# Kernel tuning notes

Measured on AMD Instinct MI355X. Metric: run time of the kernel, lower is better.

The kernel has to match this reference:

```python
import jax, jax.numpy as jnp
import numpy as np

TGT_LEN = 1024
MEM_LEN = 1024
SAME_LENGTH = True
D_MODEL = 2048
BATCH = 4


def _make_ft_real(tgt_len: int, mem_len: int, same_length: bool) -> jnp.ndarray:
    """Build the banded Fourier mixing matrix. Since the module's input x is real
    and only .real of the output is returned, Re(FT @ x) == Re(FT) @ x, so we
    precompute only the real part (this also matches the kernel-headroom note:
    the imaginary output is never used)."""
    qlen = tgt_len
    klen = tgt_len + mem_len
    flen = klen - qlen + 1
    m = np.outer(np.arange(qlen), np.arange(flen))
    ft = np.exp(2j * np.pi * m / flen) / np.sqrt(flen)  # [qlen, flen] complex
    ft = np.pad(ft, ((0, 0), (klen - flen, 0)))          # left-pad to [qlen, klen]
    for i in range(qlen):  # setup-time numpy loop over fixed qlen rows (not traced)
        ft[i] = np.roll(ft[i], -(qlen - i - 1))
    ft = np.tril(ft, klen - qlen)
    if same_length:
        ft = np.triu(ft, 0)
    return jnp.asarray(ft.real.astype(np.float32))


_FT_REAL = _make_ft_real(TGT_LEN, MEM_LEN, SAME_LENGTH)  # [tgt_len, tgt_len+mem_len]


def setup_inputs() -> dict:
    key = jax.random.key(0)
    k1, k2 = jax.random.split(key)
    klen = TGT_LEN + MEM_LEN
    x = jax.random.normal(k1, (BATCH, klen, D_MODEL), dtype=jnp.float32)
    p = jax.random.normal(k2, (BATCH, klen, D_MODEL), dtype=jnp.float32)
    return {"x": x, "p": p, "qlen": TGT_LEN, "add_position": 1}


def reference(x, p, qlen, add_position):
    # Dropout is identity in eval mode (deterministic reference).
    if add_position:
        x = x + p
    klen = x.shape[1]
    ft = _FT_REAL[-qlen:, -klen:]                    # [qlen, klen]
    scale = np.float32(1.0 / np.sqrt(klen))
    # Banded token-mixing matmul; real part only (x is real).
    out = jnp.einsum("lm,bmd->bld", ft, x) * scale   # [B, qlen, D]
    return out
```

## Files before the change

### kernel.cpp

```cpp
#include <hip/hip_runtime.h>
#include <hip/hip_bf16.h>
#include <cstdint>

#define QLEN   1024
#define KLEN   2048
#define DMODEL 2048
#define BATCH  4
#define FLEN   (KLEN - QLEN + 1)

typedef __bf16 bf16x8 __attribute__((ext_vector_type(8)));
typedef __bf16 bf16x4 __attribute__((ext_vector_type(4)));
typedef float  f32x4  __attribute__((ext_vector_type(4)));

__device__ __bf16 g_ft[(size_t)QLEN * KLEN];
__device__ __bf16 g_yt[(size_t)BATCH * DMODEL * KLEN];

typedef __attribute__((address_space(1))) void gvoid;
typedef __attribute__((address_space(3))) void svoid;

__device__ __forceinline__ void async_load16(const void* g, void* lds) {
  gvoid* gp = (gvoid*)(uintptr_t)g;
  svoid* sp = (svoid*)(uint32_t)(uintptr_t)lds;
  __builtin_amdgcn_global_load_lds(gp, sp, 16, 0, 0);
}

__global__ void gen_ft_kernel() {
  const int u  = blockIdx.x * 256 + threadIdx.x;
  const int l  = u >> 8;
  const int m0 = (u & 255) * 8;
  const int j0 = m0 - l;
  bf16x8 o = {};
  if (j0 + 7 >= 0 && j0 < FLEN) {
    const float w     = 6.283185307179586f / (float)FLEN;
    const float scale = 1.0f / sqrtf((float)FLEN * (float)KLEN);
#pragma unroll
    for (int i = 0; i < 8; ++i) {
      const int j = j0 + i;
      float v = 0.0f;
      if (j >= 0 && j < FLEN) {
        const int r = (l * j) % FLEN;
        v = cosf((float)r * w) * scale;
      }
      o[i] = (__bf16)v;
    }
  }
  *(bf16x8*)(g_ft + (size_t)u * 8) = o;
}

__global__ __launch_bounds__(256) void gen_yt_kernel(const float* __restrict__ x,
                                                     const float* __restrict__ p,
                                                     const int* __restrict__ addp) {
  __shared__ __align__(16) float xt[64 * 64];
  __shared__ __align__(16) float pt[64 * 64];
  const int b  = blockIdx.z;
  const int m0 = blockIdx.x * 64;
  const int d0 = blockIdx.y * 64;
  const int t  = threadIdx.x;
  const int lane = t & 63;
  const int wave = t >> 6;
  const float addf = (*addp) ? 1.0f : 0.0f;
  const size_t base = (size_t)b * KLEN * DMODEL;

#pragma unroll
  for (int q = 0; q < 4; ++q) {
    const int cb = q * 256 + wave * 64;
    const int fc = cb + lane;
    const int m  = fc >> 4;
    const int cl = fc & 15;
    const int gc = cl ^ ((m >> 3) & 7);
    async_load16(x + base + (size_t)(m0 + m) * DMODEL + d0 + gc * 4, xt + cb * 4);
  }
#pragma unroll
  for (int q = 0; q < 4; ++q) {
    const int cb = q * 256 + wave * 64;
    const int fc = cb + lane;
    const int m  = fc >> 4;
    const int cl = fc & 15;
    const int gc = cl ^ ((m >> 3) & 7);
    async_load16(p + base + (size_t)(m0 + m) * DMODEL + d0 + gc * 4, pt + cb * 4);
  }
  __syncthreads();

#pragma unroll
  for (int s = 0; s < 2; ++s) {
    const int u  = t + 256 * s;
    const int d  = u >> 3;
    const int mc = u & 7;
    bf16x8 o;
#pragma unroll
    for (int i = 0; i < 8; ++i) {
      const int idx = (mc * 8 + i) * 64 + 4 * ((d >> 2) ^ mc) + (d & 3);
      o[i] = (__bf16)(xt[idx] + addf * pt[idx]);
    }
    *(bf16x8*)(g_yt + base + (size_t)(d0 + d) * KLEN + (m0 + mc * 8)) = o;
  }
}

#define BM 128
#define BN 128
#define BK 64

__global__ __launch_bounds__(256) void gemm_kernel(float* __restrict__ out) {
  __shared__ __align__(16) __bf16 As[BM * BK];
  __shared__ __align__(16) __bf16 Bs[BN * BK];
  const int bn = blockIdx.x, bm = blockIdx.y, b = blockIdx.z;
  const int l0 = bm * BM, d0 = bn * BN;
  const int tid  = threadIdx.x;
  const int lane = tid & 63;
  const int wave = tid >> 6;
  const int wr = wave >> 1, wc = wave & 1;
  const int col = lane & 15, quad = lane >> 4;

  f32x4 acc[4][4] = {};

  const int t0 = l0 >> 6;
  const int t1 = (l0 + BM - 1 + FLEN - 1) >> 6;
  const __bf16* ftp = g_ft;
  const __bf16* ytp = g_yt + (size_t)b * DMODEL * KLEN;

  for (int t = t0; t <= t1; ++t) {
    const int k0 = t * BK;
#pragma unroll
    for (int s = 0; s < 4; ++s) {
      const int cb  = wave * 256 + s * 64;
      const int lc  = cb + lane;
      const int row = lc >> 3;
      const int gc8 = (lc & 7) ^ (row & 7);
      async_load16(ftp + (size_t)(l0 + row) * KLEN + k0 + gc8 * 8, As + cb * 8);
    }
#pragma unroll
    for (int s = 0; s < 4; ++s) {
      const int cb  = wave * 256 + s * 64;
      const int lc  = cb + lane;
      const int row = lc >> 3;
      const int gc8 = (lc & 7) ^ (row & 7);
      async_load16(ytp + (size_t)(d0 + row) * KLEN + k0 + gc8 * 8, Bs + cb * 8);
    }
    __syncthreads();

#pragma unroll
    for (int kk = 0; kk < 2; ++kk) {
      bf16x8 af[4], bq[4];
      const int c8 = kk * 4 + quad;
#pragma unroll
      for (int ti = 0; ti < 4; ++ti) {
        const int r = wr * 64 + ti * 16 + col;
        af[ti] = *(const bf16x8*)(As + (size_t)((r << 3) + (c8 ^ (r & 7))) * 8);
      }
#pragma unroll
      for (int tj = 0; tj < 4; ++tj) {
        const int r = wc * 64 + tj * 16 + col;
        bq[tj] = *(const bf16x8*)(Bs + (size_t)((r << 3) + (c8 ^ (r & 7))) * 8);
      }
#pragma unroll
      for (int ti = 0; ti < 4; ++ti)
#pragma unroll
        for (int tj = 0; tj < 4; ++tj)
          acc[ti][tj] = __builtin_amdgcn_mfma_f32_16x16x32_bf16(af[ti], bq[tj], acc[ti][tj], 0, 0, 0);
    }
    __syncthreads();
  }

#pragma unroll
  for (int ti = 0; ti < 4; ++ti) {
    const int l = l0 + wr * 64 + ti * 16 + quad * 4;
#pragma unroll
    for (int tj = 0; tj < 4; ++tj) {
      const int d = d0 + wc * 64 + tj * 16 + col;
      float* op = out + (size_t)b * QLEN * DMODEL + (size_t)l * DMODEL + d;
#pragma unroll
      for (int r2 = 0; r2 < 4; ++r2) op[(size_t)r2 * DMODEL] = acc[ti][tj][r2];
    }
  }
}

extern "C" void kernel_launch(void* const* d_in, const int* in_sizes, int n_in,
                              void* d_out, int out_size, void* d_ws, size_t ws_size,
                              hipStream_t stream) {
  const float* x   = (const float*)d_in[0];
  const float* p   = (const float*)d_in[1];
  const int* addp  = (const int*)d_in[3];
  float* out = (float*)d_out;

  gen_ft_kernel<<<dim3((QLEN * KLEN / 8) / 256), dim3(256), 0, stream>>>();
  gen_yt_kernel<<<dim3(KLEN / 64, DMODEL / 64, BATCH), dim3(256), 0, stream>>>(x, p, addp);
  gemm_kernel<<<dim3(DMODEL / BN, QLEN / BM, BATCH), dim3(256), 0, stream>>>(out);
}
```

Baseline: 206.2 us.

## Restructure transpose kernel into per-wave double-buffered async pipeline

```diff
diff --git a/kernel.cpp b/kernel.cpp
--- a/kernel.cpp
+++ b/kernel.cpp
@@ -50,49 +50,59 @@
 __global__ __launch_bounds__(256) void gen_yt_kernel(const float* __restrict__ x,
                                                      const float* __restrict__ p,
                                                      const int* __restrict__ addp) {
-  __shared__ __align__(16) float xt[64 * 64];
-  __shared__ __align__(16) float pt[64 * 64];
-  const int b  = blockIdx.z;
-  const int m0 = blockIdx.x * 64;
-  const int d0 = blockIdx.y * 64;
-  const int t  = threadIdx.x;
+  __shared__ __align__(16) float lds[4][2][2][512];
+  const int t    = threadIdx.x;
   const int lane = t & 63;
   const int wave = t >> 6;
   const float addf = (*addp) ? 1.0f : 0.0f;
+
+  const int W    = blockIdx.x * 4 + wave;
+  const int b    = W >> 10;
+  const int rem  = W & 1023;
+  const int mi   = rem >> 4;
+  const int m0   = mi * 32;
+  const int dw   = (rem & 15) * 128;
   const size_t base = (size_t)b * KLEN * DMODEL;
 
+  const int r_ld = lane >> 2;
+  const int q_ld = lane & 3;
+  const int d_l  = lane >> 2;
+  const int mc   = lane & 3;
+
+  auto issue = [&](int j, int bb) {
+    const int dcol = dw + j * 16;
+    float* xb = &lds[wave][bb][0][0];
+    float* pb = &lds[wave][bb][1][0];
 #pragma unroll
-  for (int q = 0; q < 4; ++q) {
-    const int cb = q * 256 + wave * 64;
-    const int fc = cb + lane;
-    const int m  = fc >> 4;
-    const int cl = fc & 15;
-    const int gc = cl ^ ((m >> 3) & 7);
-    async_load16(x + base + (size_t)(m0 + m) * DMODEL + d0 + gc * 4, xt + cb * 4);
-  }
+    for (int s = 0; s < 2; ++s) {
+      const int r = s * 16 + r_ld;
+      const size_t go = base + (size_t)(m0 + r) * DMODEL + dcol + q_ld * 4;
+      async_load16(x + go, xb + s * 256);
+      async_load16(p + go, pb + s * 256);
+    }
+  };
+
+  issue(0, 0);
 #pragma unroll
-  for (int q = 0; q < 4; ++q) {
-    const int cb = q * 256 + wave * 64;
-    const int fc = cb + lane;
-    const int m  = fc >> 4;
-    const int cl = fc & 15;
-    const int gc = cl ^ ((m >> 3) & 7);
-    async_load16(p + base + (size_t)(m0 + m) * DMODEL + d0 + gc * 4, pt + cb * 4);
-  }
-  __syncthreads();
-
-#pragma unroll
-  for (int s = 0; s < 2; ++s) {
-    const int u  = t + 256 * s;
-    const int d  = u >> 3;
-    const int mc = u & 7;
+  for (int j = 0; j < 8; ++j) {
+    if (j < 7) issue(j + 1, (j + 1) & 1);
+    if (j == 0) {
+      __builtin_amdgcn_s_waitcnt(0x0F74);
+    } else if (j < 7) {
+      __builtin_amdgcn_s_waitcnt(0x0F75);
+    } else {
+      __builtin_amdgcn_s_waitcnt(0x0F71);
+    }
+    const float* xb = &lds[wave][j & 1][0][0];
+    const float* pb = &lds[wave][j & 1][1][0];
     bf16x8 o;
 #pragma unroll
     for (int i = 0; i < 8; ++i) {
-      const int idx = (mc * 8 + i) * 64 + 4 * ((d >> 2) ^ mc) + (d & 3);
-      o[i] = (__bf16)(xt[idx] + addf * pt[idx]);
+      const int idx = (mc * 8 + i) * 16 + d_l;
+      o[i] = (__bf16)(xb[idx] + addf * pb[idx]);
     }
-    *(bf16x8*)(g_yt + base + (size_t)(d0 + d) * KLEN + (m0 + mc * 8)) = o;
+    const int dcol = dw + j * 16;
+    *(bf16x8*)(g_yt + base + (size_t)(dcol + d_l) * KLEN + (m0 + mc * 8)) = o;
   }
 }
 
@@ -183,6 +193,6 @@
   float* out = (float*)d_out;
 
   gen_ft_kernel<<<dim3((QLEN * KLEN / 8) / 256), dim3(256), 0, stream>>>();
-  gen_yt_kernel<<<dim3(KLEN / 64, DMODEL / 64, BATCH), dim3(256), 0, stream>>>(x, p, addp);
+  gen_yt_kernel<<<dim3(1024), dim3(256), 0, stream>>>(x, p, addp);
   gemm_kernel<<<dim3(DMODEL / BN, QLEN / BM, BATCH), dim3(256), 0, stream>>>(out);
 }
```

New measurement: 215.0 us. +4.3%, slower.
